# Kernel tuning notes

Hardware: AMD Instinct MI355X
Metric: run time of the kernel (lower is better)

Reference implementation:

```python
import jax, jax.numpy as jnp
import numpy as np

N = 50000      # nodes
F = 256        # input features
H = 64         # hidden
K = 2          # hops
C = 16         # classes
E1 = 800000    # 1-hop edges
E2 = 1600000   # 2-hop edges


def spmm(idx, val, r, n):
    # out[i] = sum_{e: row[e]==i} val[e] * r[col[e]]  (COO sparse-dense matmul)
    return jax.ops.segment_sum(val[:, None] * r[idx[1]], idx[0], num_segments=n)


def setup_inputs() -> dict:
    key = jax.random.key(0)
    ks = jax.random.split(key, 7)
    x = jax.random.normal(ks[0], (N, F), dtype=jnp.float32)
    a1_idx = jax.random.randint(ks[1], (2, E1), 0, N, dtype=jnp.int32)
    a1_val = jax.random.uniform(ks[2], (E1,), dtype=jnp.float32)
    a2_idx = jax.random.randint(ks[3], (2, E2), 0, N, dtype=jnp.int32)
    a2_val = jax.random.uniform(ks[4], (E2,), dtype=jnp.float32)
    w_embed = jax.random.normal(ks[5], (F, H), dtype=jnp.float32) * (2.0 / (F + H)) ** 0.5
    w_classify = jax.random.normal(ks[6], ((2 ** (K + 1) - 1) * H, C), dtype=jnp.float32) * 0.05
    return {"x": x, "a1_idx": a1_idx, "a1_val": a1_val,
            "a2_idx": a2_idx, "a2_val": a2_val,
            "w_embed": w_embed, "w_classify": w_classify}


def reference(x, a1_idx, a1_val, a2_idx, a2_val, w_embed, w_classify):
    n = x.shape[0]
    rs = [jax.nn.relu(x @ w_embed)]                       # [n, H]
    for _ in range(K):
        r = rs[-1]
        r1 = spmm(a1_idx, a1_val, r, n)
        r2 = spmm(a2_idx, a2_val, r, n)
        rs.append(jax.nn.relu(jnp.concatenate([r1, r2], axis=1)))
    r_final = jnp.concatenate(rs, axis=1)                 # [n, (2^(K+1)-1)*H]
    # dropout is identity at inference (training=False)
    logits = r_final @ w_classify                         # [n, C]
    return jax.nn.softmax(logits, axis=1)
```

## Files before the change

kernel.cpp:

```cpp
#include <hip/hip_runtime.h>
#include <hip/hip_bf16.h>
#include <hip/hip_fp16.h>


#define F_IN 256
#define H_DIM 64
#define CPAD 16
#define NS 32
#define MAXCHUNK 6272

typedef __attribute__((ext_vector_type(8))) _Float16 half8;
typedef __attribute__((ext_vector_type(4))) float f32x4;

__device__ __forceinline__ unsigned short f2h(float x) {
  return __half_as_ushort(__float2half(x));
}
__device__ __forceinline__ float h2f(unsigned u) {
  return __half2float(__ushort_as_half((unsigned short)u));
}

#define WT_LD 264
__global__ __launch_bounds__(256) void embed_mfma(
    const float* __restrict__ x, const float* __restrict__ w,
    unsigned short* __restrict__ r0h, int n) {
  __shared__ _Float16 wt[H_DIM][WT_LD];
  for (int i = threadIdx.x; i < F_IN * H_DIM / 4; i += 256) {
    float4 v = ((const float4*)w)[i];
    int k = (i * 4) >> 6;
    int c = (i * 4) & 63;
    wt[c + 0][k] = (_Float16)v.x;
    wt[c + 1][k] = (_Float16)v.y;
    wt[c + 2][k] = (_Float16)v.z;
    wt[c + 3][k] = (_Float16)v.w;
  }
  __syncthreads();
  int wid = threadIdx.x >> 6;
  int lane = threadIdx.x & 63;
  int row0 = blockIdx.x * 64 + wid * 16;
  if (row0 >= n) return;
  int arow = row0 + (lane & 15);
  int arow_c = min(arow, n - 1);
  int kbase = (lane >> 4) * 8;
  const float* xp = x + (size_t)arow_c * F_IN + kbase;
  f32x4 acc0 = (f32x4)0.f, acc1 = (f32x4)0.f, acc2 = (f32x4)0.f,
        acc3 = (f32x4)0.f;
#pragma unroll
  for (int kk = 0; kk < 8; ++kk) {
    float4 xa = *(const float4*)(xp + kk * 32);
    float4 xb = *(const float4*)(xp + kk * 32 + 4);
    half8 af;
    af[0] = (_Float16)xa.x; af[1] = (_Float16)xa.y;
    af[2] = (_Float16)xa.z; af[3] = (_Float16)xa.w;
    af[4] = (_Float16)xb.x; af[5] = (_Float16)xb.y;
    af[6] = (_Float16)xb.z; af[7] = (_Float16)xb.w;
    int kf = kk * 32 + kbase;
    half8 b0 = *(const half8*)&wt[(lane & 15) + 0][kf];
    half8 b1 = *(const half8*)&wt[(lane & 15) + 16][kf];
    half8 b2 = *(const half8*)&wt[(lane & 15) + 32][kf];
    half8 b3 = *(const half8*)&wt[(lane & 15) + 48][kf];
    acc0 = __builtin_amdgcn_mfma_f32_16x16x32_f16(af, b0, acc0, 0, 0, 0);
    acc1 = __builtin_amdgcn_mfma_f32_16x16x32_f16(af, b1, acc1, 0, 0, 0);
    acc2 = __builtin_amdgcn_mfma_f32_16x16x32_f16(af, b2, acc2, 0, 0, 0);
    acc3 = __builtin_amdgcn_mfma_f32_16x16x32_f16(af, b3, acc3, 0, 0, 0);
  }
  int drow = row0 + (lane >> 4) * 4;
#pragma unroll
  for (int i = 0; i < 4; ++i) {
    int r = drow + i;
    if (r < n) {
      unsigned short* op = &r0h[(size_t)r * H_DIM + (lane & 15)];
      op[0] = f2h(fmaxf(acc0[i], 0.f));
      op[16] = f2h(fmaxf(acc1[i], 0.f));
      op[32] = f2h(fmaxf(acc2[i], 0.f));
      op[48] = f2h(fmaxf(acc3[i], 0.f));
    }
  }
}

__global__ __launch_bounds__(256) void bucketize2(
    const int* __restrict__ i1, const float* __restrict__ v1, int E1,
    int* __restrict__ scur1, int2* __restrict__ bkt1, int sub1,
    const int* __restrict__ i2, const float* __restrict__ v2, int E2,
    int* __restrict__ scur2, int2* __restrict__ bkt2, int sub2, int PA1,
    int PAtot, int chunk) {
  int blk = blockIdx.x;
  const int* I;
  const float* V;
  int E, nb, sub;
  int* scur;
  int2* bkt;
  if (blk < PA1) {
    I = i1; V = v1; E = E1; scur = scur1; bkt = bkt1; sub = sub1; nb = PA1;
  } else {
    I = i2; V = v2; E = E2; scur = scur2; bkt = bkt2; sub = sub2;
    nb = PAtot - PA1; blk -= PA1;
  }
  int lane = threadIdx.x & 63;
  int s = blk & (NS - 1);
  for (int base_i = blk * 256; base_i < E; base_i += nb * 256) {
    int i = base_i + threadIdx.x;
    bool valid = i < E;
    int row = 0, col = 0;
    float v = 0.f;
    if (valid) {
      row = I[i];
      col = I[E + i];
      v = V[i];
    }
    int mb = valid ? (int)((unsigned)row / (unsigned)chunk) : -1;
    int2 pk;
    pk.x = row | (col << 16);
    pk.y = (int)f2h(v);
    unsigned long long mk[8];
    int mycnt = 0;
#pragma unroll
    for (int b = 0; b < 8; ++b) {
      mk[b] = __ballot(mb == b);
      if (lane == b) mycnt = (int)__popcll(mk[b]);
    }
    int mybase = 0;
    if (lane < 8 && mycnt)
      mybase = atomicAdd(&scur[(lane * NS + s) * CPAD], mycnt);
#pragma unroll
    for (int b = 0; b < 8; ++b) {
      int base = __shfl(mybase, b, 64);
      if (mb == b) {
        int rank = (int)__popcll(mk[b] & ((1ull << lane) - 1));
        bkt[(size_t)(b * NS + s) * sub + base + rank] = pk;
      }
    }
  }
}

__global__ __launch_bounds__(256) void count_stripes(
    const int* __restrict__ scur1, const int2* __restrict__ bkt1, int sub1,
    int* __restrict__ cnt1, const int* __restrict__ scur2,
    const int2* __restrict__ bkt2, int sub2, int* __restrict__ cnt2, int n,
    int chunk) {
  __shared__ int h[MAXCHUNK];
  int blk = blockIdx.x;
  int g = blk & 7;
  int s = (blk >> 3) & (NS - 1);
  int graph = blk >> 8;
  const int* scur = graph ? scur2 : scur1;
  const int2* bkt = graph ? bkt2 : bkt1;
  int sub = graph ? sub2 : sub1;
  int* cnt = graph ? cnt2 : cnt1;
  int lo = g * chunk;
  int nrows = min(n - lo, chunk);
  for (int j = threadIdx.x; j < nrows; j += 256) h[j] = 0;
  __syncthreads();
  int len = scur[(g * NS + s) * CPAD];
  const int2* bp = bkt + (size_t)(g * NS + s) * sub;
  for (int i = threadIdx.x; i < len; i += 256)
    atomicAdd(&h[(bp[i].x & 0xFFFF) - lo], 1);
  __syncthreads();
  for (int j = threadIdx.x; j < nrows; j += 256)
    cnt[(size_t)s * n + lo + j] = h[j];
}

__global__ __launch_bounds__(512) void scan_blocks2(
    const int* __restrict__ c1, int* __restrict__ e1, int* __restrict__ a1,
    unsigned short* __restrict__ so1, const int* __restrict__ c2,
    int* __restrict__ e2, int* __restrict__ a2,
    unsigned short* __restrict__ so2, int n, int NB) {
  const int* cs;
  int* exc;
  int* aux;
  unsigned short* so;
  int blk = blockIdx.x;
  if (blk < NB) {
    cs = c1; exc = e1; aux = a1; so = so1;
  } else {
    cs = c2; exc = e2; aux = a2; so = so2; blk -= NB;
  }
  __shared__ int tmp[512];
  int i = blk * 512 + threadIdx.x;
  int v = 0;
  if (i < n) {
    int acc = 0;
    unsigned off[NS];
#pragma unroll
    for (int sh = 0; sh < NS; ++sh) {
      off[sh] = (unsigned)acc;
      acc += cs[(size_t)sh * n + i];
    }
    v = acc;
#pragma unroll
    for (int q = 0; q < NS / 8; ++q) {
      uint4 st;
      st.x = off[q * 8 + 0] | (off[q * 8 + 1] << 16);
      st.y = off[q * 8 + 2] | (off[q * 8 + 3] << 16);
      st.z = off[q * 8 + 4] | (off[q * 8 + 5] << 16);
      st.w = off[q * 8 + 6] | (off[q * 8 + 7] << 16);
      *(uint4*)&so[(size_t)i * NS + q * 8] = st;
    }
  }
  tmp[threadIdx.x] = v;
  __syncthreads();
#pragma unroll
  for (int d = 1; d < 512; d <<= 1) {
    int t = (threadIdx.x >= d) ? tmp[threadIdx.x - d] : 0;
    __syncthreads();
    tmp[threadIdx.x] += t;
    __syncthreads();
  }
  if (i < n) exc[i] = tmp[threadIdx.x] - v;
  if (threadIdx.x == 511) aux[blk] = tmp[511];
}

__global__ __launch_bounds__(512) void scan_aux2(int* __restrict__ a1,
                                                 int* __restrict__ a2,
                                                 int nblk) {
  int* aux = (blockIdx.x == 0) ? a1 : a2;
  __shared__ int tmp[512];
  int v = (threadIdx.x < nblk) ? aux[threadIdx.x] : 0;
  tmp[threadIdx.x] = v;
  __syncthreads();
#pragma unroll
  for (int d = 1; d < 512; d <<= 1) {
    int t = (threadIdx.x >= d) ? tmp[threadIdx.x - d] : 0;
    __syncthreads();
    tmp[threadIdx.x] += t;
    __syncthreads();
  }
  if (threadIdx.x < nblk) aux[threadIdx.x] = tmp[threadIdx.x] - v;
}

__global__ __launch_bounds__(512) void add_offsets2(
    int* __restrict__ rs1, const int* __restrict__ a1, int E1,
    int* __restrict__ rs2, const int* __restrict__ a2, int E2, int n, int NB) {
  int blk = blockIdx.x;
  int* rs;
  const int* aux;
  int E;
  if (blk < NB) {
    rs = rs1; aux = a1; E = E1;
  } else {
    rs = rs2; aux = a2; E = E2; blk -= NB;
  }
  int i = blk * 512 + threadIdx.x;
  if (i < n) rs[i] += aux[blk];
  if (blk == 0 && threadIdx.x == 0) rs[n] = E;
}

__global__ __launch_bounds__(256) void scatter_stripes(
    const int* __restrict__ scur1, const int2* __restrict__ bkt1, int sub1,
    const int* __restrict__ rs1, const unsigned short* __restrict__ so1,
    unsigned* __restrict__ ep1, const int* __restrict__ scur2,
    const int2* __restrict__ bkt2, int sub2, const int* __restrict__ rs2,
    const unsigned short* __restrict__ so2, unsigned* __restrict__ ep2,
    int n, int chunk) {
  __shared__ int h[MAXCHUNK];
  int blk = blockIdx.x;
  int g = blk & 7;
  int s = (blk >> 3) & (NS - 1);
  int graph = blk >> 8;
  const int* scur = graph ? scur2 : scur1;
  const int2* bkt = graph ? bkt2 : bkt1;
  int sub = graph ? sub2 : sub1;
  const int* rs = graph ? rs2 : rs1;
  const unsigned short* so = graph ? so2 : so1;
  unsigned* ep = graph ? ep2 : ep1;
  int lo = g * chunk;
  int nrows = min(n - lo, chunk);
  for (int j = threadIdx.x; j < nrows; j += 256) h[j] = 0;
  __syncthreads();
  int len = scur[(g * NS + s) * CPAD];
  const int2* bp = bkt + (size_t)(g * NS + s) * sub;
  for (int i = threadIdx.x; i < len; i += 256) {
    int2 e = bp[i];
    int row = e.x & 0xFFFF;
    unsigned col = (unsigned)e.x >> 16;
    int lr = atomicAdd(&h[row - lo], 1);
    int p = rs[row] + (int)so[(size_t)row * NS + s] + lr;
    ep[p] = ((unsigned)(e.y & 0xFFFF) << 16) | col;
  }
}

__global__ __launch_bounds__(256) void spmm_h1(
    const int* __restrict__ rs1, const unsigned* __restrict__ ep1,
    const int* __restrict__ rs2, const unsigned* __restrict__ ep2,
    const unsigned short* __restrict__ r0h, unsigned short* __restrict__ r1h,
    int n, int SB) {
  const int* rs;
  const unsigned* epack;
  int coff;
  int blk = blockIdx.x;
  if (blk < SB) {
    rs = rs1; epack = ep1; coff = 0;
  } else {
    rs = rs2; epack = ep2; coff = 64; blk -= SB;
  }
  int lane = threadIdx.x & 63;
  int half = lane >> 5;
  int hl = lane & 31;
  int row = blk * 4 + (threadIdx.x >> 6);
  if (row >= n) return;
  int s = rs[row], e = rs[row + 1];
  float acc0 = 0.f, acc1 = 0.f;
  int j = s;
  for (; j + 16 <= e; j += 16) {
    unsigned pk[8];
#pragma unroll
    for (int u = 0; u < 8; ++u) pk[u] = epack[j + 2 * u + half];
    unsigned g[8];
#pragma unroll
    for (int u = 0; u < 8; ++u)
      g[u] = *(const unsigned*)&r0h[(size_t)(pk[u] & 0xFFFF) * 64 + hl * 2];
#pragma unroll
    for (int u = 0; u < 8; ++u) {
      float v = h2f(pk[u] >> 16);
      acc0 = fmaf(v, h2f(g[u] & 0xFFFF), acc0);
      acc1 = fmaf(v, h2f(g[u] >> 16), acc1);
    }
  }
  for (; j + 2 <= e; j += 2) {
    unsigned pk = epack[j + half];
    unsigned g = *(const unsigned*)&r0h[(size_t)(pk & 0xFFFF) * 64 + hl * 2];
    float v = h2f(pk >> 16);
    acc0 = fmaf(v, h2f(g & 0xFFFF), acc0);
    acc1 = fmaf(v, h2f(g >> 16), acc1);
  }
  if (j < e && half == 0) {
    unsigned pk = epack[j];
    unsigned g = *(const unsigned*)&r0h[(size_t)(pk & 0xFFFF) * 64 + hl * 2];
    float v = h2f(pk >> 16);
    acc0 = fmaf(v, h2f(g & 0xFFFF), acc0);
    acc1 = fmaf(v, h2f(g >> 16), acc1);
  }
  acc0 += __shfl_xor(acc0, 32, 64);
  acc1 += __shfl_xor(acc1, 32, 64);
  if (half == 0) {
    unsigned st = (unsigned)f2h(fmaxf(acc0, 0.f)) |
                  ((unsigned)f2h(fmaxf(acc1, 0.f)) << 16);
    *(unsigned*)&r1h[(size_t)row * 128 + coff + hl * 2] = st;
  }
}

__global__ __launch_bounds__(256) void spmm_h2(
    const int* __restrict__ rs1, const unsigned* __restrict__ ep1,
    const int* __restrict__ rs2, const unsigned* __restrict__ ep2,
    const unsigned short* __restrict__ r1h, float* __restrict__ r2, int n,
    int SB) {
  const int* rs;
  const unsigned* epack;
  int coff;
  int blk = blockIdx.x;
  if (blk < SB) {
    rs = rs1; epack = ep1; coff = 0;
  } else {
    rs = rs2; epack = ep2; coff = 128; blk -= SB;
  }
  int lane = threadIdx.x & 63;
  int half = lane >> 5;
  int hl = lane & 31;
  int row = blk * 4 + (threadIdx.x >> 6);
  if (row >= n) return;
  int s = rs[row], e = rs[row + 1];
  float acc0 = 0.f, acc1 = 0.f, acc2 = 0.f, acc3 = 0.f;
  int j = s;
  for (; j + 16 <= e; j += 16) {
    unsigned pk[8];
#pragma unroll
    for (int u = 0; u < 8; ++u) pk[u] = epack[j + 2 * u + half];
    uint2 g[8];
#pragma unroll
    for (int u = 0; u < 8; ++u)
      g[u] = *(const uint2*)&r1h[(size_t)(pk[u] & 0xFFFF) * 128 + hl * 4];
#pragma unroll
    for (int u = 0; u < 8; ++u) {
      float v = h2f(pk[u] >> 16);
      acc0 = fmaf(v, h2f(g[u].x & 0xFFFF), acc0);
      acc1 = fmaf(v, h2f(g[u].x >> 16), acc1);
      acc2 = fmaf(v, h2f(g[u].y & 0xFFFF), acc2);
      acc3 = fmaf(v, h2f(g[u].y >> 16), acc3);
    }
  }
  for (; j + 2 <= e; j += 2) {
    unsigned pk = epack[j + half];
    uint2 g = *(const uint2*)&r1h[(size_t)(pk & 0xFFFF) * 128 + hl * 4];
    float v = h2f(pk >> 16);
    acc0 = fmaf(v, h2f(g.x & 0xFFFF), acc0);
    acc1 = fmaf(v, h2f(g.x >> 16), acc1);
    acc2 = fmaf(v, h2f(g.y & 0xFFFF), acc2);
    acc3 = fmaf(v, h2f(g.y >> 16), acc3);
  }
  if (j < e && half == 0) {
    unsigned pk = epack[j];
    uint2 g = *(const uint2*)&r1h[(size_t)(pk & 0xFFFF) * 128 + hl * 4];
    float v = h2f(pk >> 16);
    acc0 = fmaf(v, h2f(g.x & 0xFFFF), acc0);
    acc1 = fmaf(v, h2f(g.x >> 16), acc1);
    acc2 = fmaf(v, h2f(g.y & 0xFFFF), acc2);
    acc3 = fmaf(v, h2f(g.y >> 16), acc3);
  }
  acc0 += __shfl_xor(acc0, 32, 64);
  acc1 += __shfl_xor(acc1, 32, 64);
  acc2 += __shfl_xor(acc2, 32, 64);
  acc3 += __shfl_xor(acc3, 32, 64);
  if (half == 0) {
    float4 st;
    st.x = fmaxf(acc0, 0.f);
    st.y = fmaxf(acc1, 0.f);
    st.z = fmaxf(acc2, 0.f);
    st.w = fmaxf(acc3, 0.f);
    *(float4*)&r2[(size_t)row * 256 + coff + hl * 4] = st;
  }
}

__global__ __launch_bounds__(256) void classify_softmax(
    const unsigned short* __restrict__ r0h,
    const unsigned short* __restrict__ r1h, const float* __restrict__ r2,
    const float* __restrict__ wc, float* __restrict__ out, int n) {
  __shared__ float wls[448 * 17];
  for (int i = threadIdx.x; i < 448 * 16; i += 256)
    wls[(i >> 4) * 17 + (i & 15)] = wc[i];
  __syncthreads();
  int lane = threadIdx.x & 63;
  int c = lane & 15;
  int part = lane >> 4;
  int node = blockIdx.x * 4 + (threadIdx.x >> 6);
  if (node >= n) return;

  float acc = 0.f;
  {
    const unsigned short* p = r0h + (size_t)node * 64 + part * 16;
#pragma unroll
    for (int j = 0; j < 2; ++j) {
      uint4 g = *(const uint4*)(p + j * 8);
      int fb = part * 16 + j * 8;
      acc = fmaf(h2f(g.x & 0xFFFF), wls[(fb + 0) * 17 + c], acc);
      acc = fmaf(h2f(g.x >> 16), wls[(fb + 1) * 17 + c], acc);
      acc = fmaf(h2f(g.y & 0xFFFF), wls[(fb + 2) * 17 + c], acc);
      acc = fmaf(h2f(g.y >> 16), wls[(fb + 3) * 17 + c], acc);
      acc = fmaf(h2f(g.z & 0xFFFF), wls[(fb + 4) * 17 + c], acc);
      acc = fmaf(h2f(g.z >> 16), wls[(fb + 5) * 17 + c], acc);
      acc = fmaf(h2f(g.w & 0xFFFF), wls[(fb + 6) * 17 + c], acc);
      acc = fmaf(h2f(g.w >> 16), wls[(fb + 7) * 17 + c], acc);
    }
  }
  {
    const unsigned short* p = r1h + (size_t)node * 128 + part * 32;
#pragma unroll
    for (int j = 0; j < 4; ++j) {
      uint4 g = *(const uint4*)(p + j * 8);
      int fb = 64 + part * 32 + j * 8;
      acc = fmaf(h2f(g.x & 0xFFFF), wls[(fb + 0) * 17 + c], acc);
      acc = fmaf(h2f(g.x >> 16), wls[(fb + 1) * 17 + c], acc);
      acc = fmaf(h2f(g.y & 0xFFFF), wls[(fb + 2) * 17 + c], acc);
      acc = fmaf(h2f(g.y >> 16), wls[(fb + 3) * 17 + c], acc);
      acc = fmaf(h2f(g.z & 0xFFFF), wls[(fb + 4) * 17 + c], acc);
      acc = fmaf(h2f(g.z >> 16), wls[(fb + 5) * 17 + c], acc);
      acc = fmaf(h2f(g.w & 0xFFFF), wls[(fb + 6) * 17 + c], acc);
      acc = fmaf(h2f(g.w >> 16), wls[(fb + 7) * 17 + c], acc);
    }
  }
  {
    const float* p = r2 + (size_t)node * 256 + part * 64;
#pragma unroll
    for (int j = 0; j < 16; ++j) {
      float4 rv = *(const float4*)(p + 4 * j);
      int fb = 192 + part * 64 + 4 * j;
      acc = fmaf(rv.x, wls[(fb + 0) * 17 + c], acc);
      acc = fmaf(rv.y, wls[(fb + 1) * 17 + c], acc);
      acc = fmaf(rv.z, wls[(fb + 2) * 17 + c], acc);
      acc = fmaf(rv.w, wls[(fb + 3) * 17 + c], acc);
    }
  }
  acc += __shfl_xor(acc, 16, 64);
  acc += __shfl_xor(acc, 32, 64);
  float m = acc;
#pragma unroll
  for (int d = 1; d < 16; d <<= 1) m = fmaxf(m, __shfl_xor(m, d, 64));
  float ex = __expf(acc - m);
  float s = ex;
#pragma unroll
  for (int d = 1; d < 16; d <<= 1) s += __shfl_xor(s, d, 64);
  if (lane < 16) out[(size_t)node * 16 + c] = ex / s;
}

extern "C" void kernel_launch(void* const* d_in, const int* in_sizes, int n_in,
                              void* d_out, int out_size, void* d_ws, size_t ws_size,
                              hipStream_t stream) {
  const float* x = (const float*)d_in[0];
  const int* a1_idx = (const int*)d_in[1];
  const float* a1_val = (const float*)d_in[2];
  const int* a2_idx = (const int*)d_in[3];
  const float* a2_val = (const float*)d_in[4];
  const float* w_embed = (const float*)d_in[5];
  const float* w_classify = (const float*)d_in[6];
  float* out = (float*)d_out;

  const int n = in_sizes[0] / F_IN;
  const int E1 = in_sizes[2];
  const int E2 = in_sizes[4];
  const int chunk = (n + 7) / 8;
  const int sub1 = E1 / (8 * NS) + 2048;
  const int sub2 = E2 / (8 * NS) + 2048;

  float* r2 = (float*)d_ws;
  unsigned short* r0h = (unsigned short*)(r2 + (size_t)n * 256);
  unsigned short* r1h = r0h + (size_t)n * 64;
  int* cnt1 = (int*)(r1h + (size_t)n * 128);
  int* cnt2 = cnt1 + (size_t)NS * n;
  int* scur = cnt2 + (size_t)NS * n;
  int* rs1 = scur + 2 * 8 * NS * CPAD;
  int* rs2 = rs1 + (n + 4);
  int* aux1 = rs2 + (n + 4);
  int* aux2 = aux1 + 512;
  unsigned short* so1 = (unsigned short*)(aux2 + 512);
  unsigned short* so2 = so1 + (size_t)NS * n;
  unsigned* ep1 = (unsigned*)(so2 + (size_t)NS * n);
  unsigned* ep2 = ep1 + E1;
  int2* bkt1 = (int2*)r2;
  int2* bkt2 = bkt1 + (size_t)8 * NS * sub1;

  auto blocks = [](long long t, int bs) { return (int)((t + bs - 1) / bs); };
  const int NB = blocks(n, 512);
  const int PA1 = 1024, PA2 = 2048;
  const int SB = blocks(n, 4);

  embed_mfma<<<blocks(n, 64), 256, 0, stream>>>(x, w_embed, r0h, n);

  hipMemsetAsync(scur, 0, 2 * 8 * NS * CPAD * sizeof(int), stream);
  bucketize2<<<PA1 + PA2, 256, 0, stream>>>(
      a1_idx, a1_val, E1, scur, bkt1, sub1, a2_idx, a2_val, E2,
      scur + 8 * NS * CPAD, bkt2, sub2, PA1, PA1 + PA2, chunk);
  count_stripes<<<2 * 8 * NS, 256, 0, stream>>>(
      scur, bkt1, sub1, cnt1, scur + 8 * NS * CPAD, bkt2, sub2, cnt2, n,
      chunk);
  scan_blocks2<<<2 * NB, 512, 0, stream>>>(cnt1, rs1, aux1, so1, cnt2, rs2,
                                           aux2, so2, n, NB);
  scan_aux2<<<2, 512, 0, stream>>>(aux1, aux2, NB);
  add_offsets2<<<2 * NB, 512, 0, stream>>>(rs1, aux1, E1, rs2, aux2, E2, n, NB);
  scatter_stripes<<<2 * 8 * NS, 256, 0, stream>>>(
      scur, bkt1, sub1, rs1, so1, ep1, scur + 8 * NS * CPAD, bkt2, sub2, rs2,
      so2, ep2, n, chunk);

  spmm_h1<<<2 * SB, 256, 0, stream>>>(rs1, ep1, rs2, ep2, r0h, r1h, n, SB);
  spmm_h2<<<2 * SB, 256, 0, stream>>>(rs1, ep1, rs2, ep2, r1h, r2, n, SB);

  classify_softmax<<<blocks(n, 4), 256, 0, stream>>>(r0h, r1h, r2, w_classify,
                                                     out, n);
}
```

Before: 304.0 us.

## Split feature tables into 32-wide slabs and partition SpMM by feature slice

Embeddings and first-hop outputs are stored as separate 32-feature slabs (64-byte rows) instead of interleaved wide rows. The SpMM kernels now launch one block group per (slab, adjacency) pair, each gathering only a narrow slice, so the per-pass gather working set is smaller and should fit in cache better. Each wave processes four edges at a time, with 16 lanes per edge and a cross-lane reduction, and edge indices are read with nontemporal loads. In exchange, the edge list is read several times (once per slab) and there are four to eight times as many blocks.

```diff
diff --git a/kernel.cpp b/kernel.cpp
--- a/kernel.cpp
+++ b/kernel.cpp
@@ -22,7 +22,7 @@
 #define WT_LD 264
 __global__ __launch_bounds__(256) void embed_mfma(
     const float* __restrict__ x, const float* __restrict__ w,
-    unsigned short* __restrict__ r0h, int n) {
+    unsigned short* __restrict__ r0s, int n) {
   __shared__ _Float16 wt[H_DIM][WT_LD];
   for (int i = threadIdx.x; i < F_IN * H_DIM / 4; i += 256) {
     float4 v = ((const float4*)w)[i];
@@ -64,15 +64,17 @@
     acc3 = __builtin_amdgcn_mfma_f32_16x16x32_f16(af, b3, acc3, 0, 0, 0);
   }
   int drow = row0 + (lane >> 4) * 4;
+  size_t sl = (size_t)n * 32;
 #pragma unroll
   for (int i = 0; i < 4; ++i) {
     int r = drow + i;
     if (r < n) {
-      unsigned short* op = &r0h[(size_t)r * H_DIM + (lane & 15)];
-      op[0] = f2h(fmaxf(acc0[i], 0.f));
-      op[16] = f2h(fmaxf(acc1[i], 0.f));
-      op[32] = f2h(fmaxf(acc2[i], 0.f));
-      op[48] = f2h(fmaxf(acc3[i], 0.f));
+      unsigned short* b0p = &r0s[(size_t)r * 32 + (lane & 15)];
+      unsigned short* b1p = b0p + sl;
+      b0p[0] = f2h(fmaxf(acc0[i], 0.f));
+      b0p[16] = f2h(fmaxf(acc1[i], 0.f));
+      b1p[0] = f2h(fmaxf(acc2[i], 0.f));
+      b1p[16] = f2h(fmaxf(acc3[i], 0.f));
     }
   }
 }
@@ -281,137 +283,91 @@
 __global__ __launch_bounds__(256) void spmm_h1(
     const int* __restrict__ rs1, const unsigned* __restrict__ ep1,
     const int* __restrict__ rs2, const unsigned* __restrict__ ep2,
-    const unsigned short* __restrict__ r0h, unsigned short* __restrict__ r1h,
+    const unsigned short* __restrict__ r0s, unsigned short* __restrict__ r1s,
     int n, int SB) {
-  const int* rs;
-  const unsigned* epack;
-  int coff;
-  int blk = blockIdx.x;
-  if (blk < SB) {
-    rs = rs1; epack = ep1; coff = 0;
-  } else {
-    rs = rs2; epack = ep2; coff = 64; blk -= SB;
-  }
+  int blk = blockIdx.x;
+  int combo = blk / SB;
+  int lblk = blk - combo * SB;
+  int p = combo >> 1, g = combo & 1;
+  const int* rs = g ? rs2 : rs1;
+  const unsigned* epack = g ? ep2 : ep1;
+  const unsigned short* tab = r0s + (size_t)p * n * 32;
+  unsigned short* outp = r1s + (size_t)(g * 2 + p) * n * 32;
   int lane = threadIdx.x & 63;
-  int half = lane >> 5;
-  int hl = lane & 31;
-  int row = blk * 4 + (threadIdx.x >> 6);
+  int eslot = lane >> 4;
+  int fl = lane & 15;
+  int row = lblk * 4 + (threadIdx.x >> 6);
   if (row >= n) return;
   int s = rs[row], e = rs[row + 1];
-  float acc0 = 0.f, acc1 = 0.f;
-  int j = s;
-  for (; j + 16 <= e; j += 16) {
-    unsigned pk[8];
-#pragma unroll
-    for (int u = 0; u < 8; ++u) pk[u] = epack[j + 2 * u + half];
-    unsigned g[8];
-#pragma unroll
-    for (int u = 0; u < 8; ++u)
-      g[u] = *(const unsigned*)&r0h[(size_t)(pk[u] & 0xFFFF) * 64 + hl * 2];
-#pragma unroll
-    for (int u = 0; u < 8; ++u) {
-      float v = h2f(pk[u] >> 16);
-      acc0 = fmaf(v, h2f(g[u] & 0xFFFF), acc0);
-      acc1 = fmaf(v, h2f(g[u] >> 16), acc1);
-    }
-  }
-  for (; j + 2 <= e; j += 2) {
-    unsigned pk = epack[j + half];
-    unsigned g = *(const unsigned*)&r0h[(size_t)(pk & 0xFFFF) * 64 + hl * 2];
-    float v = h2f(pk >> 16);
-    acc0 = fmaf(v, h2f(g & 0xFFFF), acc0);
-    acc1 = fmaf(v, h2f(g >> 16), acc1);
-  }
-  if (j < e && half == 0) {
-    unsigned pk = epack[j];
-    unsigned g = *(const unsigned*)&r0h[(size_t)(pk & 0xFFFF) * 64 + hl * 2];
-    float v = h2f(pk >> 16);
-    acc0 = fmaf(v, h2f(g & 0xFFFF), acc0);
-    acc1 = fmaf(v, h2f(g >> 16), acc1);
-  }
-  acc0 += __shfl_xor(acc0, 32, 64);
-  acc1 += __shfl_xor(acc1, 32, 64);
-  if (half == 0) {
-    unsigned st = (unsigned)f2h(fmaxf(acc0, 0.f)) |
-                  ((unsigned)f2h(fmaxf(acc1, 0.f)) << 16);
-    *(unsigned*)&r1h[(size_t)row * 128 + coff + hl * 2] = st;
+  float a0 = 0.f, a1 = 0.f;
+  for (int j = s; j < e; j += 8) {
+#pragma unroll
+    for (int d = 0; d < 2; ++d) {
+      int idx = j + d * 4 + eslot;
+      unsigned pk = idx < e ? __builtin_nontemporal_load(&epack[idx]) : 0u;
+      unsigned gv = *(const unsigned*)&tab[(size_t)(pk & 0xFFFF) * 32 + fl * 2];
+      float v = h2f(pk >> 16);
+      a0 = fmaf(v, h2f(gv & 0xFFFF), a0);
+      a1 = fmaf(v, h2f(gv >> 16), a1);
+    }
+  }
+  a0 += __shfl_xor(a0, 16, 64);
+  a0 += __shfl_xor(a0, 32, 64);
+  a1 += __shfl_xor(a1, 16, 64);
+  a1 += __shfl_xor(a1, 32, 64);
+  if (eslot == 0) {
+    unsigned st = (unsigned)f2h(fmaxf(a0, 0.f)) |
+                  ((unsigned)f2h(fmaxf(a1, 0.f)) << 16);
+    *(unsigned*)&outp[(size_t)row * 32 + fl * 2] = st;
   }
 }
 
 __global__ __launch_bounds__(256) void spmm_h2(
     const int* __restrict__ rs1, const unsigned* __restrict__ ep1,
     const int* __restrict__ rs2, const unsigned* __restrict__ ep2,
-    const unsigned short* __restrict__ r1h, float* __restrict__ r2, int n,
+    const unsigned short* __restrict__ r1s, float* __restrict__ r2, int n,
     int SB) {
-  const int* rs;
-  const unsigned* epack;
-  int coff;
-  int blk = blockIdx.x;
-  if (blk < SB) {
-    rs = rs1; epack = ep1; coff = 0;
-  } else {
-    rs = rs2; epack = ep2; coff = 128; blk -= SB;
-  }
+  int blk = blockIdx.x;
+  int combo = blk / SB;
+  int lblk = blk - combo * SB;
+  int sidx = combo >> 1, g = combo & 1;
+  const int* rs = g ? rs2 : rs1;
+  const unsigned* epack = g ? ep2 : ep1;
+  const unsigned short* tab = r1s + (size_t)sidx * n * 32;
+  int fbase = g * 128 + sidx * 32;
   int lane = threadIdx.x & 63;
-  int half = lane >> 5;
-  int hl = lane & 31;
-  int row = blk * 4 + (threadIdx.x >> 6);
+  int eslot = lane >> 4;
+  int fl = lane & 15;
+  int row = lblk * 4 + (threadIdx.x >> 6);
   if (row >= n) return;
   int s = rs[row], e = rs[row + 1];
-  float acc0 = 0.f, acc1 = 0.f, acc2 = 0.f, acc3 = 0.f;
-  int j = s;
-  for (; j + 16 <= e; j += 16) {
-    unsigned pk[8];
-#pragma unroll
-    for (int u = 0; u < 8; ++u) pk[u] = epack[j + 2 * u + half];
-    uint2 g[8];
-#pragma unroll
-    for (int u = 0; u < 8; ++u)
-      g[u] = *(const uint2*)&r1h[(size_t)(pk[u] & 0xFFFF) * 128 + hl * 4];
-#pragma unroll
-    for (int u = 0; u < 8; ++u) {
-      float v = h2f(pk[u] >> 16);
-      acc0 = fmaf(v, h2f(g[u].x & 0xFFFF), acc0);
-      acc1 = fmaf(v, h2f(g[u].x >> 16), acc1);
-      acc2 = fmaf(v, h2f(g[u].y & 0xFFFF), acc2);
-      acc3 = fmaf(v, h2f(g[u].y >> 16), acc3);
-    }
-  }
-  for (; j + 2 <= e; j += 2) {
-    unsigned pk = epack[j + half];
-    uint2 g = *(const uint2*)&r1h[(size_t)(pk & 0xFFFF) * 128 + hl * 4];
-    float v = h2f(pk >> 16);
-    acc0 = fmaf(v, h2f(g.x & 0xFFFF), acc0);
-    acc1 = fmaf(v, h2f(g.x >> 16), acc1);
-    acc2 = fmaf(v, h2f(g.y & 0xFFFF), acc2);
-    acc3 = fmaf(v, h2f(g.y >> 16), acc3);
-  }
-  if (j < e && half == 0) {
-    unsigned pk = epack[j];
-    uint2 g = *(const uint2*)&r1h[(size_t)(pk & 0xFFFF) * 128 + hl * 4];
-    float v = h2f(pk >> 16);
-    acc0 = fmaf(v, h2f(g.x & 0xFFFF), acc0);
-    acc1 = fmaf(v, h2f(g.x >> 16), acc1);
-    acc2 = fmaf(v, h2f(g.y & 0xFFFF), acc2);
-    acc3 = fmaf(v, h2f(g.y >> 16), acc3);
-  }
-  acc0 += __shfl_xor(acc0, 32, 64);
-  acc1 += __shfl_xor(acc1, 32, 64);
-  acc2 += __shfl_xor(acc2, 32, 64);
-  acc3 += __shfl_xor(acc3, 32, 64);
-  if (half == 0) {
-    float4 st;
-    st.x = fmaxf(acc0, 0.f);
-    st.y = fmaxf(acc1, 0.f);
-    st.z = fmaxf(acc2, 0.f);
-    st.w = fmaxf(acc3, 0.f);
-    *(float4*)&r2[(size_t)row * 256 + coff + hl * 4] = st;
+  float a0 = 0.f, a1 = 0.f;
+  for (int j = s; j < e; j += 8) {
+#pragma unroll
+    for (int d = 0; d < 2; ++d) {
+      int idx = j + d * 4 + eslot;
+      unsigned pk = idx < e ? __builtin_nontemporal_load(&epack[idx]) : 0u;
+      unsigned gv = *(const unsigned*)&tab[(size_t)(pk & 0xFFFF) * 32 + fl * 2];
+      float v = h2f(pk >> 16);
+      a0 = fmaf(v, h2f(gv & 0xFFFF), a0);
+      a1 = fmaf(v, h2f(gv >> 16), a1);
+    }
+  }
+  a0 += __shfl_xor(a0, 16, 64);
+  a0 += __shfl_xor(a0, 32, 64);
+  a1 += __shfl_xor(a1, 16, 64);
+  a1 += __shfl_xor(a1, 32, 64);
+  if (eslot == 0) {
+    float2 st;
+    st.x = fmaxf(a0, 0.f);
+    st.y = fmaxf(a1, 0.f);
+    *(float2*)&r2[(size_t)row * 256 + fbase + fl * 2] = st;
   }
 }
 
 __global__ __launch_bounds__(256) void classify_softmax(
-    const unsigned short* __restrict__ r0h,
-    const unsigned short* __restrict__ r1h, const float* __restrict__ r2,
+    const unsigned short* __restrict__ r0s,
+    const unsigned short* __restrict__ r1s, const float* __restrict__ r2,
     const float* __restrict__ wc, float* __restrict__ out, int n) {
   __shared__ float wls[448 * 17];
   for (int i = threadIdx.x; i < 448 * 16; i += 256)
@@ -422,10 +378,12 @@
   int part = lane >> 4;
   int node = blockIdx.x * 4 + (threadIdx.x >> 6);
   if (node >= n) return;
+  size_t sl = (size_t)n * 32;
 
   float acc = 0.f;
   {
-    const unsigned short* p = r0h + (size_t)node * 64 + part * 16;
+    const unsigned short* p =
+        r0s + (part >> 1) * sl + (size_t)node * 32 + (part & 1) * 16;
 #pragma unroll
     for (int j = 0; j < 2; ++j) {
       uint4 g = *(const uint4*)(p + j * 8);
@@ -441,7 +399,7 @@
     }
   }
   {
-    const unsigned short* p = r1h + (size_t)node * 128 + part * 32;
+    const unsigned short* p = r1s + part * sl + (size_t)node * 32;
 #pragma unroll
     for (int j = 0; j < 4; ++j) {
       uint4 g = *(const uint4*)(p + j * 8);
@@ -500,9 +458,9 @@
   const int sub2 = E2 / (8 * NS) + 2048;
 
   float* r2 = (float*)d_ws;
-  unsigned short* r0h = (unsigned short*)(r2 + (size_t)n * 256);
-  unsigned short* r1h = r0h + (size_t)n * 64;
-  int* cnt1 = (int*)(r1h + (size_t)n * 128);
+  unsigned short* r0s = (unsigned short*)(r2 + (size_t)n * 256);
+  unsigned short* r1s = r0s + (size_t)n * 64;
+  int* cnt1 = (int*)(r1s + (size_t)n * 128);
   int* cnt2 = cnt1 + (size_t)NS * n;
   int* scur = cnt2 + (size_t)NS * n;
   int* rs1 = scur + 2 * 8 * NS * CPAD;
@@ -521,7 +479,7 @@
   const int PA1 = 1024, PA2 = 2048;
   const int SB = blocks(n, 4);
 
-  embed_mfma<<<blocks(n, 64), 256, 0, stream>>>(x, w_embed, r0h, n);
+  embed_mfma<<<blocks(n, 64), 256, 0, stream>>>(x, w_embed, r0s, n);
 
   hipMemsetAsync(scur, 0, 2 * 8 * NS * CPAD * sizeof(int), stream);
   bucketize2<<<PA1 + PA2, 256, 0, stream>>>(
@@ -538,9 +496,9 @@
       scur, bkt1, sub1, rs1, so1, ep1, scur + 8 * NS * CPAD, bkt2, sub2, rs2,
       so2, ep2, n, chunk);
 
-  spmm_h1<<<2 * SB, 256, 0, stream>>>(rs1, ep1, rs2, ep2, r0h, r1h, n, SB);
-  spmm_h2<<<2 * SB, 256, 0, stream>>>(rs1, ep1, rs2, ep2, r1h, r2, n, SB);
-
-  classify_softmax<<<blocks(n, 4), 256, 0, stream>>>(r0h, r1h, r2, w_classify,
+  spmm_h1<<<4 * SB, 256, 0, stream>>>(rs1, ep1, rs2, ep2, r0s, r1s, n, SB);
+  spmm_h2<<<8 * SB, 256, 0, stream>>>(rs1, ep1, rs2, ep2, r1s, r2, n, SB);
+
+  classify_softmax<<<blocks(n, 4), 256, 0, stream>>>(r0s, r1s, r2, w_classify,
                                                      out, n);
 }
```

Result: slower. 537.1 us (+76.7%).
